# Kernel optimization log

Measured on AMD Instinct MI355X. Metric: run time of the kernel, lower is better.

Reference implementation:

```python
import jax, jax.numpy as jnp
import numpy as np

B, R, F, S, H, G, E, MH, A, TOPK = 2048, 39200, 512, 64, 512, 256, 32, 512, 7, 4


def _init(key, shape, scale=0.02):
    return (jax.random.normal(key, shape, dtype=jnp.float32) * scale).astype(jnp.float32)


def setup_inputs() -> dict:
    key = jax.random.key(0)
    ks = jax.random.split(key, 24)
    return {
        "obs": jax.random.normal(ks[0], (B, R), dtype=jnp.float32),
        "obs_sensor": jax.random.normal(ks[1], (B, S), dtype=jnp.float32),
        "std": jnp.ones((1,), dtype=jnp.float32),
        # trunk: Linear(R,F) + LayerNorm(F)
        "trunk_w": _init(ks[2], (R, F)),
        "trunk_b": jnp.zeros((F,), jnp.float32),
        "ln_g": jnp.ones((F,), jnp.float32),
        "ln_b": jnp.zeros((F,), jnp.float32),
        # policy1: Linear(F+S, H)
        "p1_w": _init(ks[3], (F + S, H)),
        "p1_b": jnp.zeros((H,), jnp.float32),
        # MoE gate MLP: Linear(H,G) -> ReLU -> Linear(G,E)
        "g_w1": _init(ks[4], (H, G)),
        "g_b1": jnp.zeros((G,), jnp.float32),
        "g_w2": _init(ks[5], (G, E)),
        "g_b2": jnp.zeros((E,), jnp.float32),
        # experts: per-expert MLP Linear(H,MH) -> ReLU -> Linear(MH,H)
        "e_w1": _init(ks[6], (E, H, MH)),
        "e_b1": jnp.zeros((E, MH), jnp.float32),
        "e_w2": _init(ks[7], (E, MH, H)),
        "e_b2": jnp.zeros((E, H), jnp.float32),
        # policy2: ReLU -> Linear(H, A)
        "p2_w": _init(ks[8], (H, A)),
        "p2_b": jnp.zeros((A,), jnp.float32),
    }


def _layernorm(x, g, b, eps=1e-5):
    mu = jnp.mean(x, axis=-1, keepdims=True)
    var = jnp.var(x, axis=-1, keepdims=True)
    return (x - mu) * jax.lax.rsqrt(var + eps) * g + b


def reference(obs, obs_sensor, std, trunk_w, trunk_b, ln_g, ln_b, p1_w, p1_b,
              g_w1, g_b1, g_w2, g_b2, e_w1, e_b1, e_w2, e_b2, p2_w, p2_b):
    # trunk
    h = jnp.tanh(_layernorm(obs @ trunk_w + trunk_b, ln_g, ln_b))
    h = jnp.concatenate([h, obs_sensor], axis=-1)
    # policy1
    x = jax.nn.relu(h @ p1_w + p1_b)  # [B, H]
    # MoE gating: top-k over softmax of gate-MLP logits
    logits = jax.nn.relu(x @ g_w1 + g_b1) @ g_w2 + g_b2  # [B, E]
    probs = jax.nn.softmax(logits, axis=-1)
    top_v, top_i = jax.lax.top_k(probs, TOPK)  # [B, K]
    w = top_v / jnp.sum(top_v, axis=-1, keepdims=True)
    rows = jnp.arange(x.shape[0])[:, None]
    gate_sparse = jnp.zeros_like(probs).at[rows, top_i].set(w)  # [B, E]
    mask = jnp.zeros_like(probs).at[rows, top_i].set(1.0)
    # expert compute (dense all-expert, weighted by sparse gate; dropout off in eval)
    hid = jax.nn.relu(jnp.einsum('bh,ehm->bem', x, e_w1) + e_b1)  # [B, E, MH]
    y = jnp.einsum('bem,emh->beh', hid, e_w2) + e_b2              # [B, E, H]
    x_moe = jnp.einsum('be,beh->bh', gate_sparse, y)              # [B, H]
    # load-balancing aux loss (Switch-style)
    density = jnp.mean(probs, axis=0)    # P_i
    frac = jnp.mean(mask, axis=0)        # f_i
    aux_loss = jnp.float32(E) * jnp.sum(frac * density)
    # policy2: ReLU -> Linear, then tanh
    mu = jnp.tanh(jax.nn.relu(x_moe) @ p2_w + p2_b)
    std_out = jnp.ones_like(mu) * std
    return (mu, std_out, aux_loss)
```

## Files before the change

### kernel.cpp

```cpp
#include <hip/hip_runtime.h>
#include <stdint.h>

typedef __attribute__((ext_vector_type(4))) float f32x4;
typedef __attribute__((ext_vector_type(8))) __bf16 bf16x8;

#define DEV __device__ __forceinline__

DEV ushort f2bf(float f) {
  union { float f; uint32_t u; } v; v.f = f;
  uint32_t u = v.u;
  return (ushort)((u + 0x7FFFu + ((u >> 16) & 1u)) >> 16);
}
DEV float bf2f(ushort h) {
  union { uint32_t u; float f; } v; v.u = ((uint32_t)h) << 16;
  return v.f;
}
DEV void async16(void* lds, const void* g) {
  __builtin_amdgcn_global_load_lds((const __attribute__((address_space(1))) void*)g,
                                   (__attribute__((address_space(3))) void*)lds, 16, 0, 0);
}

#define B_  2048
#define R_  39200
#define F_  512
#define S_  64
#define H_  512
#define G_  256
#define E_  32
#define MH_ 512
#define A_  7
#define KSLICES 7
#define KSLICE_LEN 5600

__global__ void convert_bf16_kernel(const float* __restrict__ in, ushort* __restrict__ out, long n4) {
  long i = (long)blockIdx.x * blockDim.x + threadIdx.x;
  long stride = (long)gridDim.x * blockDim.x;
  const float4* in4 = (const float4*)in;
  ushort4* out4 = (ushort4*)out;
  for (; i < n4; i += stride) {
    float4 f = in4[i];
    ushort4 o;
    o.x = f2bf(f.x); o.y = f2bf(f.y); o.z = f2bf(f.z); o.w = f2bf(f.w);
    out4[i] = o;
  }
}

__global__ void transpose_bf16_kernel(const float* __restrict__ in, ushort* __restrict__ out,
                                      int R, int C) {
  __shared__ float tile[32][33];
  size_t bo = (size_t)blockIdx.z * R * C;
  in += bo; out += bo;
  int c0 = blockIdx.x * 32, r0 = blockIdx.y * 32;
  int tx = threadIdx.x, ty = threadIdx.y;
#pragma unroll
  for (int i = 0; i < 4; i++)
    tile[ty + i*8][tx] = in[(size_t)(r0 + ty + i*8) * C + c0 + tx];
  __syncthreads();
#pragma unroll
  for (int i = 0; i < 4; i++)
    out[(size_t)(c0 + ty + i*8) * R + r0 + tx] = f2bf(tile[tx][ty + i*8]);
}

__global__ __launch_bounds__(256)
void gemm_trunk_kernel(const ushort* __restrict__ A, const ushort* __restrict__ Bt,
                       float* __restrict__ Cp) {
  __shared__ __align__(16) ushort As[128 * 32];
  __shared__ __align__(16) ushort Bs[128 * 32];
  const int tid = threadIdx.x;
  const int w = tid >> 6, l = tid & 63;
  const int wm = w >> 1, wn = w & 1;
  const int lrow = l & 15, lq = l >> 4;
  const int mb = blockIdx.x >> 2, nb = blockIdx.x & 3;
  const int ks = blockIdx.y * KSLICE_LEN;
  f32x4 acc[4][4] = {};
  const int srow = tid >> 2;
  const int scol = (tid & 3) * 8;
  const ushort* Ab = A + (size_t)(mb * 128 + srow) * R_ + scol;
  const ushort* Bb = Bt + (size_t)(nb * 128 + srow) * R_ + scol;
  char* AsB = (char*)As + w * 1024;
  char* BsB = (char*)Bs + w * 1024;
  for (int k0 = ks; k0 < ks + KSLICE_LEN; k0 += 32) {
    async16(AsB,        Ab + k0);
    async16(AsB + 4096, Ab + (size_t)64 * R_ + k0);
    async16(BsB,        Bb + k0);
    async16(BsB + 4096, Bb + (size_t)64 * R_ + k0);
    __syncthreads();
    bf16x8 af[4], bfr[4];
#pragma unroll
    for (int i = 0; i < 4; i++)
      af[i] = *(const bf16x8*)(As + (wm * 64 + i * 16 + lrow) * 32 + lq * 8);
#pragma unroll
    for (int i = 0; i < 4; i++)
      bfr[i] = *(const bf16x8*)(Bs + (wn * 64 + i * 16 + lrow) * 32 + lq * 8);
#pragma unroll
    for (int mi = 0; mi < 4; mi++)
#pragma unroll
      for (int ni = 0; ni < 4; ni++)
        acc[mi][ni] = __builtin_amdgcn_mfma_f32_16x16x32_bf16(af[mi], bfr[ni], acc[mi][ni], 0, 0, 0);
    __syncthreads();
  }
  float* C = Cp + (size_t)blockIdx.y * B_ * F_;
#pragma unroll
  for (int mi = 0; mi < 4; mi++)
#pragma unroll
    for (int ni = 0; ni < 4; ni++) {
      int col = nb * 128 + wn * 64 + ni * 16 + lrow;
#pragma unroll
      for (int r = 0; r < 4; r++) {
        int row = mb * 128 + wm * 64 + mi * 16 + lq * 4 + r;
        C[(size_t)row * F_ + col] = acc[mi][ni][r];
      }
    }
}

__global__ __launch_bounds__(256)
void gemm_brelu_kernel(const ushort* __restrict__ A, const ushort* __restrict__ Bt,
                       const float* __restrict__ bias, ushort* __restrict__ out,
                       int K, int N, int nTiles) {
  __shared__ __align__(16) ushort As[128 * 32];
  __shared__ __align__(16) ushort Bs[128 * 32];
  const int tid = threadIdx.x;
  const int w = tid >> 6, l = tid & 63;
  const int wm = w >> 1, wn = w & 1;
  const int lrow = l & 15, lq = l >> 4;
  const int mb = blockIdx.x / nTiles, nb = blockIdx.x % nTiles;
  f32x4 acc[4][4] = {};
  const int srow = tid >> 2;
  const int scol = (tid & 3) * 8;
  const ushort* Ab = A + (size_t)(mb * 128 + srow) * K + scol;
  const ushort* Bb = Bt + (size_t)(nb * 128 + srow) * K + scol;
  char* AsB = (char*)As + w * 1024;
  char* BsB = (char*)Bs + w * 1024;
  for (int k0 = 0; k0 < K; k0 += 32) {
    async16(AsB,        Ab + k0);
    async16(AsB + 4096, Ab + (size_t)64 * K + k0);
    async16(BsB,        Bb + k0);
    async16(BsB + 4096, Bb + (size_t)64 * K + k0);
    __syncthreads();
    bf16x8 af[4], bfr[4];
#pragma unroll
    for (int i = 0; i < 4; i++)
      af[i] = *(const bf16x8*)(As + (wm * 64 + i * 16 + lrow) * 32 + lq * 8);
#pragma unroll
    for (int i = 0; i < 4; i++)
      bfr[i] = *(const bf16x8*)(Bs + (wn * 64 + i * 16 + lrow) * 32 + lq * 8);
#pragma unroll
    for (int mi = 0; mi < 4; mi++)
#pragma unroll
      for (int ni = 0; ni < 4; ni++)
        acc[mi][ni] = __builtin_amdgcn_mfma_f32_16x16x32_bf16(af[mi], bfr[ni], acc[mi][ni], 0, 0, 0);
    __syncthreads();
  }
#pragma unroll
  for (int mi = 0; mi < 4; mi++)
#pragma unroll
    for (int ni = 0; ni < 4; ni++) {
      int col = nb * 128 + wn * 64 + ni * 16 + lrow;
      float bv = bias[col];
#pragma unroll
      for (int r = 0; r < 4; r++) {
        int row = mb * 128 + wm * 64 + mi * 16 + lq * 4 + r;
        out[(size_t)row * N + col] = f2bf(fmaxf(acc[mi][ni][r] + bv, 0.f));
      }
    }
}

__global__ void reduce_ln_kernel(const float* __restrict__ Cp, const float* __restrict__ tb,
                                 const float* __restrict__ g, const float* __restrict__ bb,
                                 const float* __restrict__ sensor, ushort* __restrict__ xcat) {
  int row = blockIdx.x, tid = threadIdx.x;
  const float* base = Cp + (size_t)row * F_;
  float v0 = tb[tid], v1 = tb[tid + 256];
#pragma unroll
  for (int s = 0; s < KSLICES; s++) {
    v0 += base[(size_t)s * B_ * F_ + tid];
    v1 += base[(size_t)s * B_ * F_ + tid + 256];
  }
  float s1 = v0 + v1, s2 = v0 * v0 + v1 * v1;
  for (int o = 32; o; o >>= 1) { s1 += __shfl_down(s1, o); s2 += __shfl_down(s2, o); }
  __shared__ float r1[4], r2[4];
  __shared__ float mus, rss;
  if ((tid & 63) == 0) { r1[tid >> 6] = s1; r2[tid >> 6] = s2; }
  __syncthreads();
  if (tid == 0) {
    float a = r1[0] + r1[1] + r1[2] + r1[3];
    float q = r2[0] + r2[1] + r2[2] + r2[3];
    float mu = a * (1.0f / F_);
    float var = q * (1.0f / F_) - mu * mu;
    mus = mu; rss = rsqrtf(var + 1e-5f);
  }
  __syncthreads();
  float mu = mus, rs = rss;
  ushort* xr = xcat + (size_t)row * (F_ + S_);
  xr[tid]       = f2bf(tanhf((v0 - mu) * rs * g[tid] + bb[tid]));
  xr[tid + 256] = f2bf(tanhf((v1 - mu) * rs * g[tid + 256] + bb[tid + 256]));
  if (tid < S_) xr[F_ + tid] = f2bf(sensor[(size_t)row * S_ + tid]);
}

__global__ void gate_topk_kernel(const ushort* __restrict__ tbuf, const float* __restrict__ w2,
                                 const float* __restrict__ b2, float* __restrict__ gate_w,
                                 int* __restrict__ gate_i, float* __restrict__ density,
                                 int* __restrict__ counts) {
  int row = blockIdx.x, tid = threadIdx.x;
  int jj = tid >> 5, e = tid & 31;
  const ushort* tr = tbuf + (size_t)row * G_;
  float s = 0;
  int k0 = jj * 32;
#pragma unroll
  for (int k = 0; k < 32; k++) s += bf2f(tr[k0 + k]) * w2[(size_t)(k0 + k) * E_ + e];
  __shared__ float part[8][32];
  part[jj][e] = s;
  __syncthreads();
  if (tid < 32) {
    float logit = b2[tid];
#pragma unroll
    for (int j = 0; j < 8; j++) logit += part[j][tid];
    float m = logit;
    for (int o = 16; o; o >>= 1) m = fmaxf(m, __shfl_xor(m, o));
    float p = expf(logit - m);
    float sum = p;
    for (int o = 16; o; o >>= 1) sum += __shfl_xor(sum, o);
    float prob = p / sum;
    bool sel = false;
    float tv[4]; int ti[4];
#pragma unroll
    for (int it = 0; it < 4; it++) {
      float c = sel ? -1.0f : prob;
      float mx = c;
      for (int o = 16; o; o >>= 1) mx = fmaxf(mx, __shfl_xor(mx, o));
      unsigned long long bal = __ballot(c == mx);
      int idx = __ffsll(bal) - 1;
      if (tid == idx) sel = true;
      tv[it] = mx; ti[it] = idx;
    }
    float wsum = tv[0] + tv[1] + tv[2] + tv[3];
#pragma unroll
    for (int it = 0; it < 4; it++)
      if (tid == it) { gate_w[row * 4 + it] = tv[it] / wsum; gate_i[row * 4 + it] = ti[it]; }
    atomicAdd(&density[tid], prob);
    if (sel) atomicAdd(&counts[tid], 1);
  }
}

__global__ void scan_aux_kernel(const int* __restrict__ counts, const float* __restrict__ density,
                                int* __restrict__ offsets, float* __restrict__ aux_out) {
  if (threadIdx.x == 0) {
    int acc = 0; float a = 0;
    for (int e = 0; e < E_; e++) {
      offsets[e] = acc; acc += counts[e];
      a += (float)counts[e] * density[e];
    }
    aux_out[0] = (float)E_ * a / ((float)B_ * (float)B_);
  }
}

__global__ void fill_slots_kernel(const int* __restrict__ gate_i, const float* __restrict__ gate_w,
                                  const int* __restrict__ offsets, int* __restrict__ cursors,
                                  int* __restrict__ slot_row, float* __restrict__ slot_w) {
  int r = blockIdx.x * blockDim.x + threadIdx.x;
  if (r >= B_) return;
  for (int k = 0; k < 4; k++) {
    int e = gate_i[r * 4 + k];
    int pos = atomicAdd(&cursors[e], 1);
    int s = offsets[e] + pos;
    slot_row[s] = r;
    slot_w[s] = gate_w[r * 4 + k];
  }
}

__global__ __launch_bounds__(256)
void expert1_kernel(const ushort* __restrict__ x, const ushort* __restrict__ w1T,
                    const float* __restrict__ b1, const int* __restrict__ counts,
                    const int* __restrict__ offsets, const int* __restrict__ slot_row,
                    ushort* __restrict__ hid) {
  const int e = blockIdx.z, nb = blockIdx.y, cx = blockIdx.x;
  const int cnt = counts[e];
  if (cnt == 0) return;
  const int off = offsets[e];
  __shared__ __align__(16) ushort As[64 * 32];
  __shared__ __align__(16) ushort Bs[128 * 32];
  const int tid = threadIdx.x;
  const int w = tid >> 6, l = tid & 63;
  const int wm = w >> 1, wn = w & 1;
  const int lrow = l & 15, lq = l >> 4;
  const int srow = tid >> 2, scol = (tid & 3) * 8;
  const ushort* Wb = w1T + (size_t)e * H_ * MH_ + (size_t)(nb * 128 + srow) * H_ + scol;
  char* AsB = (char*)As + w * 1024;
  char* BsB = (char*)Bs + w * 1024;
  for (int base = cx * 64; base < cnt; base += 64 * 8) {
    int sl = base + srow; if (sl > cnt - 1) sl = cnt - 1;
    const ushort* Ab = x + (size_t)slot_row[off + sl] * H_ + scol;
    f32x4 acc[2][4] = {};
    for (int k0 = 0; k0 < H_; k0 += 32) {
      async16(AsB,        Ab + k0);
      async16(BsB,        Wb + k0);
      async16(BsB + 4096, Wb + (size_t)64 * H_ + k0);
      __syncthreads();
      bf16x8 af[2], bfr[4];
#pragma unroll
      for (int i = 0; i < 2; i++)
        af[i] = *(const bf16x8*)(As + (wm * 32 + i * 16 + lrow) * 32 + lq * 8);
#pragma unroll
      for (int i = 0; i < 4; i++)
        bfr[i] = *(const bf16x8*)(Bs + (wn * 64 + i * 16 + lrow) * 32 + lq * 8);
#pragma unroll
      for (int mi = 0; mi < 2; mi++)
#pragma unroll
        for (int ni = 0; ni < 4; ni++)
          acc[mi][ni] = __builtin_amdgcn_mfma_f32_16x16x32_bf16(af[mi], bfr[ni], acc[mi][ni], 0, 0, 0);
      __syncthreads();
    }
    int mrem = cnt - base;
#pragma unroll
    for (int mi = 0; mi < 2; mi++)
#pragma unroll
      for (int ni = 0; ni < 4; ni++) {
        int col = nb * 128 + wn * 64 + ni * 16 + lrow;
        float bv = b1[e * MH_ + col];
#pragma unroll
        for (int r = 0; r < 4; r++) {
          int rl = wm * 32 + mi * 16 + lq * 4 + r;
          if (rl < mrem)
            hid[(size_t)(off + base + rl) * MH_ + col] = f2bf(fmaxf(acc[mi][ni][r] + bv, 0.f));
        }
      }
  }
}

__global__ __launch_bounds__(256)
void expert2_kernel(const ushort* __restrict__ hid, const ushort* __restrict__ w2T,
                    const float* __restrict__ b2, const int* __restrict__ counts,
                    const int* __restrict__ offsets, const int* __restrict__ slot_row,
                    const float* __restrict__ slot_w, float* __restrict__ xmoe) {
  const int e = blockIdx.z, nb = blockIdx.y, cx = blockIdx.x;
  const int cnt = counts[e];
  if (cnt == 0) return;
  const int off = offsets[e];
  __shared__ __align__(16) ushort As[64 * 32];
  __shared__ __align__(16) ushort Bs[128 * 32];
  const int tid = threadIdx.x;
  const int w = tid >> 6, l = tid & 63;
  const int wm = w >> 1, wn = w & 1;
  const int lrow = l & 15, lq = l >> 4;
  const int srow = tid >> 2, scol = (tid & 3) * 8;
  const ushort* Wb = w2T + (size_t)e * MH_ * H_ + (size_t)(nb * 128 + srow) * MH_ + scol;
  char* AsB = (char*)As + w * 1024;
  char* BsB = (char*)Bs + w * 1024;
  for (int base = cx * 64; base < cnt; base += 64 * 8) {
    int sl = base + srow; if (sl > cnt - 1) sl = cnt - 1;
    const ushort* Ab = hid + (size_t)(off + sl) * MH_ + scol;
    f32x4 acc[2][4] = {};
    for (int k0 = 0; k0 < MH_; k0 += 32) {
      async16(AsB,        Ab + k0);
      async16(BsB,        Wb + k0);
      async16(BsB + 4096, Wb + (size_t)64 * MH_ + k0);
      __syncthreads();
      bf16x8 af[2], bfr[4];
#pragma unroll
      for (int i = 0; i < 2; i++)
        af[i] = *(const bf16x8*)(As + (wm * 32 + i * 16 + lrow) * 32 + lq * 8);
#pragma unroll
      for (int i = 0; i < 4; i++)
        bfr[i] = *(const bf16x8*)(Bs + (wn * 64 + i * 16 + lrow) * 32 + lq * 8);
#pragma unroll
      for (int mi = 0; mi < 2; mi++)
#pragma unroll
        for (int ni = 0; ni < 4; ni++)
          acc[mi][ni] = __builtin_amdgcn_mfma_f32_16x16x32_bf16(af[mi], bfr[ni], acc[mi][ni], 0, 0, 0);
      __syncthreads();
    }
    int mrem = cnt - base;
#pragma unroll
    for (int mi = 0; mi < 2; mi++)
#pragma unroll
      for (int ni = 0; ni < 4; ni++) {
        int col = nb * 128 + wn * 64 + ni * 16 + lrow;
        float bv = b2[e * H_ + col];
#pragma unroll
        for (int r = 0; r < 4; r++) {
          int rl = wm * 32 + mi * 16 + lq * 4 + r;
          if (rl < mrem) {
            int s = off + base + rl;
            atomicAdd(&xmoe[(size_t)slot_row[s] * H_ + col], slot_w[s] * (acc[mi][ni][r] + bv));
          }
        }
      }
  }
}

__global__ void policy2_kernel(const float* __restrict__ xm, const float* __restrict__ w,
                               const float* __restrict__ b, const float* __restrict__ stdp,
                               float* __restrict__ out) {
  int l = threadIdx.x & 63;
  int row = blockIdx.x * 4 + (threadIdx.x >> 6);
  const float* xr = xm + (size_t)row * H_;
  const float4* x4 = (const float4*)(xr + l * 8);
  float4 a0 = x4[0], a1 = x4[1];
  float v[8] = {a0.x, a0.y, a0.z, a0.w, a1.x, a1.y, a1.z, a1.w};
#pragma unroll
  for (int j = 0; j < 8; j++) v[j] = fmaxf(v[j], 0.f);
  float res[7];
#pragma unroll
  for (int a = 0; a < A_; a++) {
    float s = 0;
#pragma unroll
    for (int j = 0; j < 8; j++) s += v[j] * w[(size_t)(l * 8 + j) * A_ + a];
    for (int o = 32; o; o >>= 1) s += __shfl_down(s, o);
    res[a] = s;
  }
  if (l == 0) {
    float sv = stdp[0];
#pragma unroll
    for (int a = 0; a < A_; a++) {
      out[(size_t)row * A_ + a] = tanhf(res[a] + b[a]);
      out[(size_t)B_ * A_ + (size_t)row * A_ + a] = sv;
    }
  }
}

extern "C" void kernel_launch(void* const* d_in, const int* in_sizes, int n_in,
                              void* d_out, int out_size, void* d_ws, size_t ws_size,
                              hipStream_t stream) {
  const float* obs      = (const float*)d_in[0];
  const float* sensor   = (const float*)d_in[1];
  const float* stdp     = (const float*)d_in[2];
  const float* trunk_w  = (const float*)d_in[3];
  const float* trunk_b  = (const float*)d_in[4];
  const float* ln_g     = (const float*)d_in[5];
  const float* ln_b     = (const float*)d_in[6];
  const float* p1_w     = (const float*)d_in[7];
  const float* p1_b     = (const float*)d_in[8];
  const float* g_w1     = (const float*)d_in[9];
  const float* g_b1     = (const float*)d_in[10];
  const float* g_w2     = (const float*)d_in[11];
  const float* g_b2     = (const float*)d_in[12];
  const float* e_w1     = (const float*)d_in[13];
  const float* e_b1     = (const float*)d_in[14];
  const float* e_w2     = (const float*)d_in[15];
  const float* e_b2     = (const float*)d_in[16];
  const float* p2_w     = (const float*)d_in[17];
  const float* p2_b     = (const float*)d_in[18];
  float* out = (float*)d_out;

  char* ws = (char*)d_ws;
  size_t off = 0;
  auto alloc = [&](size_t bytes) -> char* {
    char* p = ws + off;
    off += (bytes + 255) & ~(size_t)255;
    return p;
  };
  ushort* obs_bf  = (ushort*)alloc((size_t)B_ * R_ * 2);
  ushort* wT      = (ushort*)alloc((size_t)F_ * R_ * 2);
  float*  partial = (float*) alloc((size_t)KSLICES * B_ * F_ * 4);
  ushort* xcat    = (ushort*)alloc((size_t)B_ * (F_ + S_) * 2);
  ushort* p1T     = (ushort*)alloc((size_t)H_ * (F_ + S_) * 2);
  ushort* xbuf    = (ushort*)alloc((size_t)B_ * H_ * 2);
  ushort* g1T     = (ushort*)alloc((size_t)G_ * H_ * 2);
  ushort* tbuf    = (ushort*)alloc((size_t)B_ * G_ * 2);
  ushort* ew1T    = (ushort*)alloc((size_t)E_ * H_ * MH_ * 2);
  ushort* ew2T    = (ushort*)alloc((size_t)E_ * MH_ * H_ * 2);
  ushort* hid     = (ushort*)alloc(((size_t)B_ * 4 + 64) * MH_ * 2);
  float*  xmoe    = (float*) alloc((size_t)B_ * H_ * 4);
  float*  gate_w  = (float*) alloc((size_t)B_ * 4 * 4);
  int*    gate_i  = (int*)   alloc((size_t)B_ * 4 * 4);
  int*    counts  = (int*)   alloc(E_ * 4);
  int*    offsets = (int*)   alloc(E_ * 4);
  int*    cursors = (int*)   alloc(E_ * 4);
  float*  density = (float*) alloc(E_ * 4);
  int*    slot_row= (int*)   alloc((size_t)B_ * 4 * 4);
  float*  slot_w  = (float*) alloc((size_t)B_ * 4 * 4);

  hipMemsetAsync(counts, 0, E_ * 4, stream);
  hipMemsetAsync(cursors, 0, E_ * 4, stream);
  hipMemsetAsync(density, 0, E_ * 4, stream);
  hipMemsetAsync(xmoe, 0, (size_t)B_ * H_ * 4, stream);

  convert_bf16_kernel<<<8192, 256, 0, stream>>>(obs, obs_bf, (long)B_ * R_ / 4);
  transpose_bf16_kernel<<<dim3(F_/32, R_/32, 1),  dim3(32, 8), 0, stream>>>(trunk_w, wT, R_, F_);
  transpose_bf16_kernel<<<dim3(H_/32, (F_+S_)/32, 1), dim3(32, 8), 0, stream>>>(p1_w, p1T, F_ + S_, H_);
  transpose_bf16_kernel<<<dim3(G_/32, H_/32, 1),  dim3(32, 8), 0, stream>>>(g_w1, g1T, H_, G_);
  transpose_bf16_kernel<<<dim3(MH_/32, H_/32, E_), dim3(32, 8), 0, stream>>>(e_w1, ew1T, H_, MH_);
  transpose_bf16_kernel<<<dim3(H_/32, MH_/32, E_), dim3(32, 8), 0, stream>>>(e_w2, ew2T, MH_, H_);

  gemm_trunk_kernel<<<dim3(64, KSLICES), 256, 0, stream>>>(obs_bf, wT, partial);
  reduce_ln_kernel<<<B_, 256, 0, stream>>>(partial, trunk_b, ln_g, ln_b, sensor, xcat);

  gemm_brelu_kernel<<<16 * 4, 256, 0, stream>>>(xcat, p1T, p1_b, xbuf, F_ + S_, H_, 4);
  gemm_brelu_kernel<<<16 * 2, 256, 0, stream>>>(xbuf, g1T, g_b1, tbuf, H_, G_, 2);
  gate_topk_kernel<<<B_, 256, 0, stream>>>(tbuf, g_w2, g_b2, gate_w, gate_i, density, counts);
  scan_aux_kernel<<<1, 64, 0, stream>>>(counts, density, offsets, out + 2 * B_ * A_);
  fill_slots_kernel<<<8, 256, 0, stream>>>(gate_i, gate_w, offsets, cursors, slot_row, slot_w);

  expert1_kernel<<<dim3(8, 4, E_), 256, 0, stream>>>(xbuf, ew1T, e_b1, counts, offsets, slot_row, hid);
  expert2_kernel<<<dim3(8, 4, E_), 256, 0, stream>>>(hid, ew2T, e_b2, counts, offsets, slot_row, slot_w, xmoe);

  policy2_kernel<<<B_ / 4, 256, 0, stream>>>(xmoe, p2_w, p2_b, stdp, out);
}
```

Baseline: 1.026 ms.

## Fuse obs bf16 conversion into trunk GEMM, retile small GEMMs and transposes

```diff
diff --git a/kernel.cpp b/kernel.cpp
--- a/kernel.cpp
+++ b/kernel.cpp
@@ -3,15 +3,17 @@
 
 typedef __attribute__((ext_vector_type(4))) float f32x4;
 typedef __attribute__((ext_vector_type(8))) __bf16 bf16x8;
+typedef unsigned short u16;
+typedef u16 u16x8 __attribute__((ext_vector_type(8)));
 
 #define DEV __device__ __forceinline__
 
-DEV ushort f2bf(float f) {
+DEV u16 f2bf(float f) {
   union { float f; uint32_t u; } v; v.f = f;
   uint32_t u = v.u;
-  return (ushort)((u + 0x7FFFu + ((u >> 16) & 1u)) >> 16);
-}
-DEV float bf2f(ushort h) {
+  return (u16)((u + 0x7FFFu + ((u >> 16) & 1u)) >> 16);
+}
+DEV float bf2f(u16 h) {
   union { uint32_t u; float f; } v; v.u = ((uint32_t)h) << 16;
   return v.f;
 }
@@ -29,40 +31,52 @@
 #define E_  32
 #define MH_ 512
 #define A_  7
-#define KSLICES 7
-#define KSLICE_LEN 5600
-
-__global__ void convert_bf16_kernel(const float* __restrict__ in, ushort* __restrict__ out, long n4) {
-  long i = (long)blockIdx.x * blockDim.x + threadIdx.x;
-  long stride = (long)gridDim.x * blockDim.x;
-  const float4* in4 = (const float4*)in;
-  ushort4* out4 = (ushort4*)out;
-  for (; i < n4; i += stride) {
-    float4 f = in4[i];
-    ushort4 o;
-    o.x = f2bf(f.x); o.y = f2bf(f.y); o.z = f2bf(f.z); o.w = f2bf(f.w);
-    out4[i] = o;
-  }
-}
+#define KSLICES 35
+#define KSLICE_LEN 1120
 
 __global__ void transpose_bf16_kernel(const float* __restrict__ in, ushort* __restrict__ out,
                                       int R, int C) {
-  __shared__ float tile[32][33];
+  __shared__ float tile[64][65];
   size_t bo = (size_t)blockIdx.z * R * C;
-  in += bo; out += bo;
-  int c0 = blockIdx.x * 32, r0 = blockIdx.y * 32;
-  int tx = threadIdx.x, ty = threadIdx.y;
-#pragma unroll
-  for (int i = 0; i < 4; i++)
-    tile[ty + i*8][tx] = in[(size_t)(r0 + ty + i*8) * C + c0 + tx];
+  const float* inp = in + bo;
+  ushort* outp = out + bo;
+  int r0 = blockIdx.y * 64, c0 = blockIdx.x * 64;
+  int tid = threadIdx.x;
+  {
+    int rl = tid >> 2, cl = (tid & 3) * 16;
+    if (r0 + rl < R) {
+      const float4* src = (const float4*)(inp + (size_t)(r0 + rl) * C + c0 + cl);
+#pragma unroll
+      for (int j = 0; j < 4; j++) {
+        float4 v = src[j];
+        tile[rl][cl + 4 * j + 0] = v.x;
+        tile[rl][cl + 4 * j + 1] = v.y;
+        tile[rl][cl + 4 * j + 2] = v.z;
+        tile[rl][cl + 4 * j + 3] = v.w;
+      }
+    }
+  }
   __syncthreads();
-#pragma unroll
-  for (int i = 0; i < 4; i++)
-    out[(size_t)(c0 + ty + i*8) * R + r0 + tx] = f2bf(tile[tx][ty + i*8]);
+  {
+    int cl = tid >> 2, rl = (tid & 3) * 16;
+    ushort* dst = outp + (size_t)(c0 + cl) * R + r0 + rl;
+#pragma unroll
+    for (int j = 0; j < 4; j++) {
+      int rr = rl + 4 * j;
+      if (r0 + rr < R) {
+        ushort4 o;
+        o.x = f2bf(tile[rr + 0][cl]);
+        o.y = f2bf(tile[rr + 1][cl]);
+        o.z = f2bf(tile[rr + 2][cl]);
+        o.w = f2bf(tile[rr + 3][cl]);
+        *(ushort4*)(dst + 4 * j) = o;
+      }
+    }
+  }
 }
 
 __global__ __launch_bounds__(256)
-void gemm_trunk_kernel(const ushort* __restrict__ A, const ushort* __restrict__ Bt,
+void gemm_trunk_kernel(const float* __restrict__ A, const ushort* __restrict__ Bt,
                        float* __restrict__ Cp) {
   __shared__ __align__(16) ushort As[128 * 32];
   __shared__ __align__(16) ushort Bs[128 * 32];
@@ -73,17 +87,24 @@
   const int mb = blockIdx.x >> 2, nb = blockIdx.x & 3;
   const int ks = blockIdx.y * KSLICE_LEN;
   f32x4 acc[4][4] = {};
-  const int srow = tid >> 2;
-  const int scol = (tid & 3) * 8;
-  const ushort* Ab = A + (size_t)(mb * 128 + srow) * R_ + scol;
+  const int srow = tid >> 2, scol = (tid & 3) * 8;
   const ushort* Bb = Bt + (size_t)(nb * 128 + srow) * R_ + scol;
-  char* AsB = (char*)As + w * 1024;
   char* BsB = (char*)Bs + w * 1024;
+  const int arow = tid >> 1, acol = (tid & 1) * 16;
+  const float* Ap = A + (size_t)(mb * 128 + arow) * R_ + acol;
+  ushort* AsW = As + arow * 32 + acol;
   for (int k0 = ks; k0 < ks + KSLICE_LEN; k0 += 32) {
-    async16(AsB,        Ab + k0);
-    async16(AsB + 4096, Ab + (size_t)64 * R_ + k0);
     async16(BsB,        Bb + k0);
     async16(BsB + 4096, Bb + (size_t)64 * R_ + k0);
+    const float4* av = (const float4*)(Ap + k0);
+    float4 f0 = av[0], f1 = av[1], f2 = av[2], f3 = av[3];
+    u16x8 p0, p1;
+    p0[0]=f2bf(f0.x); p0[1]=f2bf(f0.y); p0[2]=f2bf(f0.z); p0[3]=f2bf(f0.w);
+    p0[4]=f2bf(f1.x); p0[5]=f2bf(f1.y); p0[6]=f2bf(f1.z); p0[7]=f2bf(f1.w);
+    p1[0]=f2bf(f2.x); p1[1]=f2bf(f2.y); p1[2]=f2bf(f2.z); p1[3]=f2bf(f2.w);
+    p1[4]=f2bf(f3.x); p1[5]=f2bf(f3.y); p1[6]=f2bf(f3.z); p1[7]=f2bf(f3.w);
+    *(u16x8*)AsW       = p0;
+    *(u16x8*)(AsW + 8) = p1;
     __syncthreads();
     bf16x8 af[4], bfr[4];
 #pragma unroll
@@ -114,52 +135,49 @@
 }
 
 __global__ __launch_bounds__(256)
-void gemm_brelu_kernel(const ushort* __restrict__ A, const ushort* __restrict__ Bt,
-                       const float* __restrict__ bias, ushort* __restrict__ out,
-                       int K, int N, int nTiles) {
-  __shared__ __align__(16) ushort As[128 * 32];
-  __shared__ __align__(16) ushort Bs[128 * 32];
+void gemm64_brelu_kernel(const ushort* __restrict__ A, const ushort* __restrict__ Bt,
+                         const float* __restrict__ bias, ushort* __restrict__ out,
+                         int K, int N, int nTiles) {
+  __shared__ __align__(16) ushort As[64 * 32];
+  __shared__ __align__(16) ushort Bs[64 * 32];
   const int tid = threadIdx.x;
   const int w = tid >> 6, l = tid & 63;
   const int wm = w >> 1, wn = w & 1;
   const int lrow = l & 15, lq = l >> 4;
   const int mb = blockIdx.x / nTiles, nb = blockIdx.x % nTiles;
-  f32x4 acc[4][4] = {};
-  const int srow = tid >> 2;
-  const int scol = (tid & 3) * 8;
-  const ushort* Ab = A + (size_t)(mb * 128 + srow) * K + scol;
-  const ushort* Bb = Bt + (size_t)(nb * 128 + srow) * K + scol;
+  f32x4 acc[2][2] = {};
+  const int srow = tid >> 2, scol = (tid & 3) * 8;
+  const ushort* Ab = A + (size_t)(mb * 64 + srow) * K + scol;
+  const ushort* Bb = Bt + (size_t)(nb * 64 + srow) * K + scol;
   char* AsB = (char*)As + w * 1024;
   char* BsB = (char*)Bs + w * 1024;
   for (int k0 = 0; k0 < K; k0 += 32) {
-    async16(AsB,        Ab + k0);
-    async16(AsB + 4096, Ab + (size_t)64 * K + k0);
-    async16(BsB,        Bb + k0);
-    async16(BsB + 4096, Bb + (size_t)64 * K + k0);
+    async16(AsB, Ab + k0);
+    async16(BsB, Bb + k0);
     __syncthreads();
-    bf16x8 af[4], bfr[4];
-#pragma unroll
-    for (int i = 0; i < 4; i++)
-      af[i] = *(const bf16x8*)(As + (wm * 64 + i * 16 + lrow) * 32 + lq * 8);
-#pragma unroll
-    for (int i = 0; i < 4; i++)
-      bfr[i] = *(const bf16x8*)(Bs + (wn * 64 + i * 16 + lrow) * 32 + lq * 8);
-#pragma unroll
-    for (int mi = 0; mi < 4; mi++)
-#pragma unroll
-      for (int ni = 0; ni < 4; ni++)
+    bf16x8 af[2], bfr[2];
+#pragma unroll
+    for (int i = 0; i < 2; i++)
+      af[i] = *(const bf16x8*)(As + (wm * 32 + i * 16 + lrow) * 32 + lq * 8);
+#pragma unroll
+    for (int i = 0; i < 2; i++)
+      bfr[i] = *(const bf16x8*)(Bs + (wn * 32 + i * 16 + lrow) * 32 + lq * 8);
+#pragma unroll
+    for (int mi = 0; mi < 2; mi++)
+#pragma unroll
+      for (int ni = 0; ni < 2; ni++)
         acc[mi][ni] = __builtin_amdgcn_mfma_f32_16x16x32_bf16(af[mi], bfr[ni], acc[mi][ni], 0, 0, 0);
     __syncthreads();
   }
 #pragma unroll
-  for (int mi = 0; mi < 4; mi++)
-#pragma unroll
-    for (int ni = 0; ni < 4; ni++) {
-      int col = nb * 128 + wn * 64 + ni * 16 + lrow;
+  for (int mi = 0; mi < 2; mi++)
+#pragma unroll
+    for (int ni = 0; ni < 2; ni++) {
+      int col = nb * 64 + wn * 32 + ni * 16 + lrow;
       float bv = bias[col];
 #pragma unroll
       for (int r = 0; r < 4; r++) {
-        int row = mb * 128 + wm * 64 + mi * 16 + lq * 4 + r;
+        int row = mb * 64 + wm * 32 + mi * 16 + lq * 4 + r;
         out[(size_t)row * N + col] = f2bf(fmaxf(acc[mi][ni][r] + bv, 0.f));
       }
     }
@@ -202,12 +220,21 @@
                                  int* __restrict__ gate_i, float* __restrict__ density,
                                  int* __restrict__ counts) {
   int row = blockIdx.x, tid = threadIdx.x;
+  __shared__ float trs[G_];
+  const ushort* tr = tbuf + (size_t)row * G_;
+  if (tid < 64) {
+    ushort4 v = ((const ushort4*)tr)[tid];
+    trs[tid * 4 + 0] = bf2f(v.x);
+    trs[tid * 4 + 1] = bf2f(v.y);
+    trs[tid * 4 + 2] = bf2f(v.z);
+    trs[tid * 4 + 3] = bf2f(v.w);
+  }
+  __syncthreads();
   int jj = tid >> 5, e = tid & 31;
-  const ushort* tr = tbuf + (size_t)row * G_;
   float s = 0;
   int k0 = jj * 32;
 #pragma unroll
-  for (int k = 0; k < 32; k++) s += bf2f(tr[k0 + k]) * w2[(size_t)(k0 + k) * E_ + e];
+  for (int k = 0; k < 32; k++) s += trs[k0 + k] * w2[(size_t)(k0 + k) * E_ + e];
   __shared__ float part[8][32];
   part[jj][e] = s;
   __syncthreads();
@@ -449,7 +476,6 @@
     off += (bytes + 255) & ~(size_t)255;
     return p;
   };
-  ushort* obs_bf  = (ushort*)alloc((size_t)B_ * R_ * 2);
   ushort* wT      = (ushort*)alloc((size_t)F_ * R_ * 2);
   float*  partial = (float*) alloc((size_t)KSLICES * B_ * F_ * 4);
   ushort* xcat    = (ushort*)alloc((size_t)B_ * (F_ + S_) * 2);
@@ -475,18 +501,17 @@
   hipMemsetAsync(density, 0, E_ * 4, stream);
   hipMemsetAsync(xmoe, 0, (size_t)B_ * H_ * 4, stream);
 
-  convert_bf16_kernel<<<8192, 256, 0, stream>>>(obs, obs_bf, (long)B_ * R_ / 4);
-  transpose_bf16_kernel<<<dim3(F_/32, R_/32, 1),  dim3(32, 8), 0, stream>>>(trunk_w, wT, R_, F_);
-  transpose_bf16_kernel<<<dim3(H_/32, (F_+S_)/32, 1), dim3(32, 8), 0, stream>>>(p1_w, p1T, F_ + S_, H_);
-  transpose_bf16_kernel<<<dim3(G_/32, H_/32, 1),  dim3(32, 8), 0, stream>>>(g_w1, g1T, H_, G_);
-  transpose_bf16_kernel<<<dim3(MH_/32, H_/32, E_), dim3(32, 8), 0, stream>>>(e_w1, ew1T, H_, MH_);
-  transpose_bf16_kernel<<<dim3(H_/32, MH_/32, E_), dim3(32, 8), 0, stream>>>(e_w2, ew2T, MH_, H_);
-
-  gemm_trunk_kernel<<<dim3(64, KSLICES), 256, 0, stream>>>(obs_bf, wT, partial);
+  transpose_bf16_kernel<<<dim3(F_/64, (R_+63)/64, 1),   dim3(256), 0, stream>>>(trunk_w, wT, R_, F_);
+  transpose_bf16_kernel<<<dim3(H_/64, (F_+S_)/64, 1),   dim3(256), 0, stream>>>(p1_w, p1T, F_ + S_, H_);
+  transpose_bf16_kernel<<<dim3(G_/64, H_/64, 1),        dim3(256), 0, stream>>>(g_w1, g1T, H_, G_);
+  transpose_bf16_kernel<<<dim3(MH_/64, H_/64, E_),      dim3(256), 0, stream>>>(e_w1, ew1T, H_, MH_);
+  transpose_bf16_kernel<<<dim3(H_/64, MH_/64, E_),      dim3(256), 0, stream>>>(e_w2, ew2T, MH_, H_);
+
+  gemm_trunk_kernel<<<dim3(64, KSLICES), 256, 0, stream>>>(obs, wT, partial);
   reduce_ln_kernel<<<B_, 256, 0, stream>>>(partial, trunk_b, ln_g, ln_b, sensor, xcat);
 
-  gemm_brelu_kernel<<<16 * 4, 256, 0, stream>>>(xcat, p1T, p1_b, xbuf, F_ + S_, H_, 4);
-  gemm_brelu_kernel<<<16 * 2, 256, 0, stream>>>(xbuf, g1T, g_b1, tbuf, H_, G_, 2);
+  gemm64_brelu_kernel<<<32 * 8, 256, 0, stream>>>(xcat, p1T, p1_b, xbuf, F_ + S_, H_, 8);
+  gemm64_brelu_kernel<<<32 * 4, 256, 0, stream>>>(xbuf, g1T, g_b1, tbuf, H_, G_, 4);
   gate_topk_kernel<<<B_, 256, 0, stream>>>(tbuf, g_w2, g_b2, gate_w, gate_i, density, counts);
   scan_aux_kernel<<<1, 64, 0, stream>>>(counts, density, offsets, out + 2 * B_ * A_);
   fill_slots_kernel<<<8, 256, 0, stream>>>(gate_i, gate_w, offsets, cursors, slot_row, slot_w);
```

New measurement: 985.8 us. 3.9% less time.
